# Optimization experiments

Measured on AMD Instinct MI355X. Metric: run time of the kernel, lower is better.

The kernel has to match this reference:

```python
import jax, jax.numpy as jnp
import numpy as np

N_DRUG = 572
EMB = 512
K_NB = 64
SEG_NB = 16
BN_EPS = 1e-5


def setup_inputs() -> dict:
    key = jax.random.key(0)
    ks = jax.random.split(key, 8)
    return {
        "drug_name": jnp.arange(N_DRUG, dtype=jnp.int64) if jax.config.jax_enable_x64 else jnp.arange(N_DRUG, dtype=jnp.int32),
        "adj_tail": jax.random.randint(ks[0], (N_DRUG, K_NB), 0, 100000),
        "adj_relation": jax.random.randint(ks[1], (N_DRUG, K_NB), 0, 200),
        "inv_adj_idx": jax.random.randint(ks[2], (N_DRUG, SEG_NB), 0, N_DRUG),
        "drug_table": jax.random.normal(ks[3], (N_DRUG, EMB), dtype=jnp.float32),
        "rela_table": jax.random.normal(ks[4], (200, EMB), dtype=jnp.float32),
        "ent_table": jax.random.normal(ks[5], (100000, EMB), dtype=jnp.float32),
        "W_lin": jax.random.normal(ks[6], (2 * EMB, EMB), dtype=jnp.float32) * (1.0 / np.sqrt(2 * EMB)),
        "b_lin": jnp.zeros((EMB,), jnp.float32),
        "bn_gamma": jnp.ones((EMB,), jnp.float32),
        "bn_beta": jnp.zeros((EMB,), jnp.float32),
        "epoch": 2,
    }


def _forward(drug_name, adj_tail, adj_relation, inv_adj_idx,
             drug_table, rela_table, ent_table, W_lin, b_lin,
             bn_gamma, bn_beta, epoch):
    # Embedding gathers
    drug_emb = drug_table[drug_name]          # [N, D]
    rel_emb = rela_table[adj_relation]        # [N, K, D]
    ent_emb = ent_table[adj_tail]             # [N, K, D]

    # KGCN-style attention over sampled neighbors: score_k = softmax(drug . rel_k)
    scores = jax.nn.softmax(jnp.einsum('nd,nkd->nk', drug_emb, rel_emb), axis=1)
    attended = jnp.einsum('nk,nkd->nd', scores, ent_emb)  # [N, D]

    # Linear -> ReLU -> BatchNorm1d (training-mode batch stats, biased var)
    e = jnp.concatenate([attended, drug_emb], axis=1)     # [N, 2D]
    h = jax.nn.relu(e @ W_lin + b_lin)                    # [N, D]
    mu = jnp.mean(h, axis=0)
    var = jnp.mean(jnp.square(h - mu), axis=0)
    drug_f = bn_gamma * (h - mu) * jax.lax.rsqrt(var + BN_EPS) + bn_beta

    if epoch > 1:
        # Sequential in-place neighbor averaging (faithful to the Python loop:
        # later drugs see already-updated rows).
        def body(f, x):
            i, pos = x
            avg = jnp.mean(f[pos], axis=0)                # [D]
            f = f.at[i].set((avg + f[i]) * 0.5)
            return f, None
        idxs = jnp.arange(N_DRUG)
        drug_f, _ = jax.lax.scan(body, drug_f, (idxs, inv_adj_idx))
    return drug_f


def reference(drug_name, adj_tail, adj_relation, inv_adj_idx,
              drug_table, rela_table, ent_table, W_lin, b_lin,
              bn_gamma, bn_beta, epoch):
    return _forward(drug_name, adj_tail, adj_relation, inv_adj_idx,
                    drug_table, rela_table, ent_table, W_lin, b_lin,
                    bn_gamma, bn_beta, epoch)
```

## Files before the change

kernel.cpp:

```cpp
#include <hip/hip_runtime.h>
#include <hip/hip_bf16.h>

#define N_DRUG 572
#define EMB    512
#define K_NB   64
#define SEG_NB 16
#define SCOLS  16

typedef __hip_bfloat16  bf16;
typedef __hip_bfloat162 bf162;

__device__ __forceinline__ float b2f(bf16 x){ return __bfloat162float(x); }

template<typename T> __device__ __forceinline__ float ldf(const T* p);
template<> __device__ __forceinline__ float ldf<float>(const float* p){ return *p; }
template<> __device__ __forceinline__ float ldf<bf16>(const bf16* p){ return b2f(*p); }

template<typename T> __device__ __forceinline__ float2 ld2(const T* p);
template<> __device__ __forceinline__ float2 ld2<float>(const float* p){ return *(const float2*)p; }
template<> __device__ __forceinline__ float2 ld2<bf16>(const bf16* p){
    bf162 v = *(const bf162*)p; return make_float2(b2f(v.x), b2f(v.y));
}

template<typename T> __device__ __forceinline__ void st2(T* p, float x, float y);
template<> __device__ __forceinline__ void st2<float>(float* p, float x, float y){ *(float2*)p = make_float2(x, y); }
template<> __device__ __forceinline__ void st2<bf16>(bf16* p, float x, float y){
    bf162 v; v.x = __float2bfloat16(x); v.y = __float2bfloat16(y); *(bf162*)p = v;
}

__device__ __forceinline__ bool idx_is64(const void* drug_name) {
    return ((const int*)drug_name)[1] == 0;
}
__device__ __forceinline__ int ld_idx(const void* p, int i, bool is64) {
    return is64 ? (int)((const long long*)p)[i] : ((const int*)p)[i];
}

__device__ __forceinline__ bool detect_bf16(const void* tab) {
    const int lane = threadIdx.x & 63;
    int hit = 0;
    if (lane < 32) {
        const unsigned u = ((const unsigned*)tab)[lane * 997];
        const unsigned e = (u >> 7) & 0xffu;
        hit = (e >= 110u && e <= 141u) ? 1 : 0;
    }
    return __popcll(__ballot(hit)) >= 24;
}

struct __align__(16) FwdSmem {
    float e[2][2 * EMB];
    float sc[2][K_NB];
    int   tl[2][K_NB];
};

template<typename T>
__device__ void fwd_impl(FwdSmem& sm,
    const void* drug_name, const void* adj_tail, const void* adj_rel,
    const T* __restrict__ drug_table, const T* __restrict__ rela_table,
    const T* __restrict__ ent_table,  const T* __restrict__ W,
    const T* __restrict__ bl, T* __restrict__ h)
{
    const int  t    = threadIdx.x;
    const int  n0   = blockIdx.x * 2;
    const bool is64 = idx_is64(drug_name);

    #pragma unroll
    for (int dr = 0; dr < 2; ++dr) {
        const int row = ld_idx(drug_name, n0 + dr, is64);
        const float2 v = ld2(drug_table + (size_t)row * EMB + 2 * t);
        sm.e[dr][EMB + 2 * t]     = v.x;
        sm.e[dr][EMB + 2 * t + 1] = v.y;
    }
    if (t < 128) {
        const int dr = t >> 6, k = t & 63;
        sm.tl[dr][k] = ld_idx(adj_tail, (n0 + dr) * K_NB + k, is64);
    }
    __syncthreads();

    {
        const int wave = t >> 6, lane = t & 63;
        const int dr = wave >> 1;
        const int kb = (wave & 1) * 32;
        const float* ed = &sm.e[dr][EMB];
        #pragma unroll 4
        for (int i = 0; i < 32; ++i) {
            const int k   = kb + i;
            const int rid = ld_idx(adj_rel, (n0 + dr) * K_NB + k, is64);
            const T* rl = rela_table + (size_t)rid * EMB;
            float p = 0.f;
            #pragma unroll
            for (int m = 0; m < 4; ++m) {
                const int dd = 2 * lane + m * 128;
                const float2 rv = ld2(rl + dd);
                p = fmaf(ed[dd],     rv.x, p);
                p = fmaf(ed[dd + 1], rv.y, p);
            }
            #pragma unroll
            for (int off = 32; off; off >>= 1) p += __shfl_down(p, off, 64);
            if (lane == 0) sm.sc[dr][k] = p;
        }
    }
    __syncthreads();

    if (t < 128) {
        const int dr = t >> 6, k = t & 63;
        const float s = sm.sc[dr][k];
        float m = s;
        #pragma unroll
        for (int off = 32; off; off >>= 1) m = fmaxf(m, __shfl_xor(m, off, 64));
        const float ex = __expf(s - m);
        float sum = ex;
        #pragma unroll
        for (int off = 32; off; off >>= 1) sum += __shfl_xor(sum, off, 64);
        sm.sc[dr][k] = ex / sum;
    }
    __syncthreads();

    {
        float a00 = 0.f, a01 = 0.f, a10 = 0.f, a11 = 0.f;
        #pragma unroll 4
        for (int k = 0; k < K_NB; ++k) {
            const float w0 = sm.sc[0][k], w1 = sm.sc[1][k];
            const float2 v0 = ld2(ent_table + (size_t)sm.tl[0][k] * EMB + 2 * t);
            const float2 v1 = ld2(ent_table + (size_t)sm.tl[1][k] * EMB + 2 * t);
            a00 = fmaf(w0, v0.x, a00); a01 = fmaf(w0, v0.y, a01);
            a10 = fmaf(w1, v1.x, a10); a11 = fmaf(w1, v1.y, a11);
        }
        sm.e[0][2 * t] = a00; sm.e[0][2 * t + 1] = a01;
        sm.e[1][2 * t] = a10; sm.e[1][2 * t + 1] = a11;
    }
    __syncthreads();

    {
        const int d0 = 2 * t;
        const float2 bb = ld2(bl + d0);
        float a00 = bb.x, a01 = bb.y, a10 = bb.x, a11 = bb.y;
        const float4* E0 = (const float4*)&sm.e[0][0];
        const float4* E1 = (const float4*)&sm.e[1][0];
        #pragma unroll 2
        for (int q = 0; q < (2 * EMB) / 4; ++q) {
            const float4 f0 = E0[q];
            const float4 f1 = E1[q];
            const T* Wp = W + (size_t)(4 * q) * EMB + d0;
            const float2 w0 = ld2(Wp);
            const float2 w1 = ld2(Wp + EMB);
            const float2 w2 = ld2(Wp + 2 * EMB);
            const float2 w3 = ld2(Wp + 3 * EMB);
            a00 = fmaf(f0.x, w0.x, a00); a01 = fmaf(f0.x, w0.y, a01);
            a10 = fmaf(f1.x, w0.x, a10); a11 = fmaf(f1.x, w0.y, a11);
            a00 = fmaf(f0.y, w1.x, a00); a01 = fmaf(f0.y, w1.y, a01);
            a10 = fmaf(f1.y, w1.x, a10); a11 = fmaf(f1.y, w1.y, a11);
            a00 = fmaf(f0.z, w2.x, a00); a01 = fmaf(f0.z, w2.y, a01);
            a10 = fmaf(f1.z, w2.x, a10); a11 = fmaf(f1.z, w2.y, a11);
            a00 = fmaf(f0.w, w3.x, a00); a01 = fmaf(f0.w, w3.y, a01);
            a10 = fmaf(f1.w, w3.x, a10); a11 = fmaf(f1.w, w3.y, a11);
        }
        st2(h + (size_t)n0 * EMB + d0,       fmaxf(a00, 0.f), fmaxf(a01, 0.f));
        st2(h + (size_t)(n0 + 1) * EMB + d0, fmaxf(a10, 0.f), fmaxf(a11, 0.f));
    }
}

__global__ __launch_bounds__(256) void k_fwd(
    const void* drug_name, const void* adj_tail, const void* adj_rel,
    const void* drug_tab, const void* rela_tab, const void* ent_tab,
    const void* W, const void* bl, void* h)
{
    __shared__ FwdSmem sm;
    if (detect_bf16(drug_tab))
        fwd_impl<bf16>(sm, drug_name, adj_tail, adj_rel,
                       (const bf16*)drug_tab, (const bf16*)rela_tab,
                       (const bf16*)ent_tab, (const bf16*)W,
                       (const bf16*)bl, (bf16*)h);
    else
        fwd_impl<float>(sm, drug_name, adj_tail, adj_rel,
                        (const float*)drug_tab, (const float*)rela_tab,
                        (const float*)ent_tab, (const float*)W,
                        (const float*)bl, (float*)h);
}

struct __align__(16) ScanSmem {
    float    fbuf[N_DRUG * SCOLS];
    unsigned obuf[N_DRUG * SEG_NB];
    float2   corr[576];
};

__device__ __forceinline__ float bflo(unsigned u){ return __uint_as_float(u << 16); }
__device__ __forceinline__ float bfhi(unsigned u){ return __uint_as_float(u & 0xffff0000u); }
__device__ __forceinline__ unsigned pack_bf2(float a, float b) {
    bf162 v; v.x = __float2bfloat16(a); v.y = __float2bfloat16(b);
    unsigned u; __builtin_memcpy(&u, &v, 4); return u;
}

template<typename T>
__device__ __forceinline__ void stage_fbuf(float* fbuf, const T* h, int c0, int t);
template<>
__device__ __forceinline__ void stage_fbuf<float>(float* fbuf, const float* h, int c0, int t) {
    float4* dst = (float4*)fbuf;
    #pragma unroll 4
    for (int k = t; k < N_DRUG * 4; k += 64)
        dst[k] = *(const float4*)(h + (size_t)(k >> 2) * EMB + c0 + 4 * (k & 3));
}
template<>
__device__ __forceinline__ void stage_fbuf<bf16>(float* fbuf, const bf16* h, int c0, int t) {
    float4* dst = (float4*)fbuf;
    #pragma unroll 4
    for (int k = t; k < N_DRUG * 2; k += 64) {
        const uint4 v = *(const uint4*)(h + (size_t)(k >> 1) * EMB + c0 + 8 * (k & 1));
        dst[2 * k]     = make_float4(bflo(v.x), bfhi(v.x), bflo(v.y), bfhi(v.y));
        dst[2 * k + 1] = make_float4(bflo(v.z), bfhi(v.z), bflo(v.w), bfhi(v.w));
    }
}

template<typename T>
__device__ __forceinline__ void flush_fbuf(const float* fbuf, T* h, int c0, int t);
template<>
__device__ __forceinline__ void flush_fbuf<float>(const float* fbuf, float* h, int c0, int t) {
    const float4* src = (const float4*)fbuf;
    #pragma unroll 4
    for (int k = t; k < N_DRUG * 4; k += 64)
        *(float4*)(h + (size_t)(k >> 2) * EMB + c0 + 4 * (k & 3)) = src[k];
}
template<>
__device__ __forceinline__ void flush_fbuf<bf16>(const float* fbuf, bf16* h, int c0, int t) {
    const float4* src = (const float4*)fbuf;
    #pragma unroll 4
    for (int k = t; k < N_DRUG * 2; k += 64) {
        const float4 f0 = src[2 * k], f1 = src[2 * k + 1];
        uint4 o;
        o.x = pack_bf2(f0.x, f0.y); o.y = pack_bf2(f0.z, f0.w);
        o.z = pack_bf2(f1.x, f1.y); o.w = pack_bf2(f1.z, f1.w);
        *(uint4*)(h + (size_t)(k >> 1) * EMB + c0 + 8 * (k & 1)) = o;
    }
}

template<bool IS64>
__device__ __forceinline__ void stage_obuf(unsigned* obuf, const void* inv, int t) {
    const uint4* src = (const uint4*)inv;
    if (IS64) {
        #pragma unroll 4
        for (int k = t; k < (N_DRUG * SEG_NB) / 2; k += 64) {
            const uint4 v = src[k];
            *(uint2*)(obuf + 2 * k) = make_uint2(v.x << 4, v.z << 4);
        }
    } else {
        uint4* dst = (uint4*)obuf;
        #pragma unroll 4
        for (int k = t; k < (N_DRUG * SEG_NB) / 4; k += 64) {
            uint4 v = src[k];
            v.x <<= 4; v.y <<= 4; v.z <<= 4; v.w <<= 4;
            dst[k] = v;
        }
    }
}

#define LD_OFF(OF, R)                                                        \
    {                                                                        \
        const uint4 q0 = ob4[(R) * 4 + 0], q1 = ob4[(R) * 4 + 1];            \
        const uint4 q2 = ob4[(R) * 4 + 2], q3 = ob4[(R) * 4 + 3];            \
        OF[0]=q0.x; OF[1]=q0.y; OF[2]=q0.z; OF[3]=q0.w;                      \
        OF[4]=q1.x; OF[5]=q1.y; OF[6]=q1.z; OF[7]=q1.w;                      \
        OF[8]=q2.x; OF[9]=q2.y; OF[10]=q2.z; OF[11]=q2.w;                    \
        OF[12]=q3.x; OF[13]=q3.y; OF[14]=q3.z; OF[15]=q3.w;                  \
    }

#define SCAN_ROW(V, OF, fi, cc, I, IP2, IP4)                                 \
    {                                                                        \
        const float s0 = (V[0] + V[1]) + (V[2] + V[3]);                      \
        const float s1 = (V[4] + V[5]) + (V[6] + V[7]);                      \
        const float s2 = (V[8] + V[9]) + (V[10] + V[11]);                    \
        const float s3 = (V[12] + V[13]) + (V[14] + V[15]);                  \
        float nv = fmaf((s0 + s1) + (s2 + s3), 1.f / 32.f, fi * 0.5f);       \
        nv = fmaf(cc.x, nv1 - f1, nv);                                       \
        nv = fmaf(cc.y, nv2 - f2, nv);                                       \
        f2 = f1; f1 = fi; nv2 = nv1; nv1 = nv;                               \
        _Pragma("unroll")                                                    \
        for (int j = 0; j < 16; ++j) V[j] = fb[OF[j]];                       \
        fi = fb[(IP2) * 16];                                                 \
        cc = sm.corr[(I) + 2];                                               \
        sm.fbuf[(I) * SCOLS + t] = nv;                                       \
        LD_OFF(OF, IP4);                                                     \
    }

template<typename T, bool IS64>
__device__ void scan_impl(ScanSmem& sm, T* __restrict__ h,
    const void* __restrict__ inv, const T* __restrict__ gamma,
    const T* __restrict__ beta, const void* __restrict__ epoch)
{
    const int t  = threadIdx.x;
    const int c0 = blockIdx.x * SCOLS;

    stage_obuf<IS64>(sm.obuf, inv, t);
    stage_fbuf<T>(sm.fbuf, h, c0, t);
    for (int k = t; k < 576; k += 64) sm.corr[k] = make_float2(0.f, 0.f);
    __syncthreads();

    for (int i = 1 + t; i < N_DRUG; i += 64) {
        const unsigned tA = (unsigned)(i - 1) << 4;
        const unsigned tB = (unsigned)(i - 2) << 4;
        int cA = 0, cB = 0;
        #pragma unroll
        for (int j = 0; j < SEG_NB; ++j) {
            const unsigned o = sm.obuf[i * SEG_NB + j];
            cA += (o == tA) ? 1 : 0;
            cB += (o == tB) ? 1 : 0;
        }
        sm.corr[i] = make_float2((float)cA * (1.f / 32.f), (float)cB * (1.f / 32.f));
    }

    {
        const int c = t & 15, g = t >> 4;
        float s = 0.f, s2 = 0.f;
        for (int r = g; r < N_DRUG; r += 4) {
            const float x = sm.fbuf[r * SCOLS + c];
            s += x; s2 = fmaf(x, x, s2);
        }
        s  += __shfl_xor(s, 16, 64);  s  += __shfl_xor(s, 32, 64);
        s2 += __shfl_xor(s2, 16, 64); s2 += __shfl_xor(s2, 32, 64);
        const float mu  = s * (1.f / N_DRUG);
        const float var = fmaxf(s2 * (1.f / N_DRUG) - mu * mu, 0.f);
        const float gs  = ldf(gamma + c0 + c) * rsqrtf(var + 1e-5f);
        const float bs  = ldf(beta  + c0 + c);
        for (int r = g; r < N_DRUG; r += 4) {
            const float x = sm.fbuf[r * SCOLS + c];
            sm.fbuf[r * SCOLS + c] = fmaf(x - mu, gs, bs);
        }
    }
    __syncthreads();

    if (((const int*)epoch)[0] > 1 && t < 16) {
        const float* fb  = sm.fbuf + t;
        const uint4* ob4 = (const uint4*)sm.obuf;

        unsigned OFA[16], OFB[16];
        float    VA[16],  VB[16];

        LD_OFF(OFA, 0); LD_OFF(OFB, 1);
        #pragma unroll
        for (int j = 0; j < 16; ++j) VA[j] = fb[OFA[j]];
        #pragma unroll
        for (int j = 0; j < 16; ++j) VB[j] = fb[OFB[j]];
        LD_OFF(OFA, 2); LD_OFF(OFB, 3);
        float  fiA = fb[0],        fiB = fb[16];
        float2 ccA = sm.corr[0],   ccB = sm.corr[1];
        float nv1 = 0.f, nv2 = 0.f, f1 = 0.f, f2 = 0.f;

        for (int i = 0; i < N_DRUG; i += 2) {
            const int a2 = (i + 2 < N_DRUG) ? i + 2 : N_DRUG - 1;
            const int a4 = (i + 4 < N_DRUG) ? i + 4 : N_DRUG - 1;
            SCAN_ROW(VA, OFA, fiA, ccA, i, a2, a4);
            const int b2 = (i + 3 < N_DRUG) ? i + 3 : N_DRUG - 1;
            const int b4 = (i + 5 < N_DRUG) ? i + 5 : N_DRUG - 1;
            SCAN_ROW(VB, OFB, fiB, ccB, i + 1, b2, b4);
        }
    }
    __syncthreads();

    flush_fbuf<T>(sm.fbuf, h, c0, t);
}

__global__ __launch_bounds__(64) void k_scan(
    void* h, const void* inv, const void* gamma, const void* beta,
    const void* epoch, const void* drug_name, const void* drug_tab)
{
    __shared__ ScanSmem sm;
    const bool isbf = detect_bf16(drug_tab);
    const bool is64 = idx_is64(drug_name);
    if (isbf) {
        if (is64) scan_impl<bf16, true >(sm, (bf16*)h, inv, (const bf16*)gamma, (const bf16*)beta, epoch);
        else      scan_impl<bf16, false>(sm, (bf16*)h, inv, (const bf16*)gamma, (const bf16*)beta, epoch);
    } else {
        if (is64) scan_impl<float, true >(sm, (float*)h, inv, (const float*)gamma, (const float*)beta, epoch);
        else      scan_impl<float, false>(sm, (float*)h, inv, (const float*)gamma, (const float*)beta, epoch);
    }
}

extern "C" void kernel_launch(void* const* d_in, const int* in_sizes, int n_in,
                              void* d_out, int out_size, void* d_ws, size_t ws_size,
                              hipStream_t stream)
{
    (void)in_sizes; (void)n_in; (void)out_size; (void)d_ws; (void)ws_size;

    k_fwd<<<N_DRUG / 2, 256, 0, stream>>>(
        d_in[0], d_in[1], d_in[2],
        d_in[4], d_in[5], d_in[6],
        d_in[7], d_in[8],
        d_out);
    k_scan<<<EMB / SCOLS, 64, 0, stream>>>(
        d_out, d_in[3],
        d_in[9], d_in[10], d_in[11],
        d_in[0], d_in[4]);
}
```

Before: 496.7 us.

## Spread sequential neighbor-averaging scan across four lane groups with shuffle reduction

The serial neighbor-averaging scan previously ran on 16 lanes, each loading and summing all 16 neighbor values per row. It now uses all 64 lanes: each group of 16 lanes gathers 4 of the neighbors and the partial sums are combined with two cross-lane shuffles. The software pipeline is reworked to a 4-row rotation with deeper prefetch of offsets, self values and correction terms. This shortens the per-row serial dependency chain of loads and adds, at the cost of shuffle latency on the critical path.

```diff
diff --git a/kernel.cpp b/kernel.cpp
--- a/kernel.cpp
+++ b/kernel.cpp
@@ -252,32 +252,21 @@
     }
 }
 
-#define LD_OFF(OF, R)                                                        \
+#define BODY(Vc, Vn, Qn, Fc, Cc, I)                                          \
     {                                                                        \
-        const uint4 q0 = ob4[(R) * 4 + 0], q1 = ob4[(R) * 4 + 1];            \
-        const uint4 q2 = ob4[(R) * 4 + 2], q3 = ob4[(R) * 4 + 3];            \
-        OF[0]=q0.x; OF[1]=q0.y; OF[2]=q0.z; OF[3]=q0.w;                      \
-        OF[4]=q1.x; OF[5]=q1.y; OF[6]=q1.z; OF[7]=q1.w;                      \
-        OF[8]=q2.x; OF[9]=q2.y; OF[10]=q2.z; OF[11]=q2.w;                    \
-        OF[12]=q3.x; OF[13]=q3.y; OF[14]=q3.z; OF[15]=q3.w;                  \
-    }
-
-#define SCAN_ROW(V, OF, fi, cc, I, IP2, IP4)                                 \
-    {                                                                        \
-        const float s0 = (V[0] + V[1]) + (V[2] + V[3]);                      \
-        const float s1 = (V[4] + V[5]) + (V[6] + V[7]);                      \
-        const float s2 = (V[8] + V[9]) + (V[10] + V[11]);                    \
-        const float s3 = (V[12] + V[13]) + (V[14] + V[15]);                  \
-        float nv = fmaf((s0 + s1) + (s2 + s3), 1.f / 32.f, fi * 0.5f);       \
-        nv = fmaf(cc.x, nv1 - f1, nv);                                       \
-        nv = fmaf(cc.y, nv2 - f2, nv);                                       \
-        f2 = f1; f1 = fi; nv2 = nv1; nv1 = nv;                               \
-        _Pragma("unroll")                                                    \
-        for (int j = 0; j < 16; ++j) V[j] = fb[OF[j]];                       \
-        fi = fb[(IP2) * 16];                                                 \
-        cc = sm.corr[(I) + 2];                                               \
-        sm.fbuf[(I) * SCOLS + t] = nv;                                       \
-        LD_OFF(OF, IP4);                                                     \
+        Vn.x = fb[Qn.x + c]; Vn.y = fb[Qn.y + c];                            \
+        Vn.z = fb[Qn.z + c]; Vn.w = fb[Qn.w + c];                            \
+        Qn = ob4[(((I) + 6 <= N_DRUG - 1) ? (I) + 6 : N_DRUG - 1) * 4 + g];  \
+        float s = (Vc.x + Vc.y) + (Vc.z + Vc.w);                             \
+        s += __shfl_xor(s, 16, 64);                                          \
+        s += __shfl_xor(s, 32, 64);                                          \
+        float nv = fmaf(s, 1.f / 32.f, Fc * 0.5f);                           \
+        nv = fmaf(Cc.x, nv1 - f1, nv);                                       \
+        nv = fmaf(Cc.y, nv2 - f2, nv);                                       \
+        f2 = f1; f1 = Fc; nv2 = nv1; nv1 = nv;                               \
+        Fc = fb[(((I) + 4 <= N_DRUG - 1) ? (I) + 4 : N_DRUG - 1) * 16 + c];  \
+        Cc = sm.corr[(I) + 4];                                               \
+        if (g == 0) sm.fbuf[(I) * SCOLS + c] = nv;                           \
     }
 
 template<typename T, bool IS64>
@@ -326,30 +315,36 @@
     }
     __syncthreads();
 
-    if (((const int*)epoch)[0] > 1 && t < 16) {
-        const float* fb  = sm.fbuf + t;
+    if (((const int*)epoch)[0] > 1) {
+        const int c = t & 15, g = t >> 4;
+        const float* fb  = sm.fbuf;
         const uint4* ob4 = (const uint4*)sm.obuf;
 
-        unsigned OFA[16], OFB[16];
-        float    VA[16],  VB[16];
-
-        LD_OFF(OFA, 0); LD_OFF(OFB, 1);
-        #pragma unroll
-        for (int j = 0; j < 16; ++j) VA[j] = fb[OFA[j]];
-        #pragma unroll
-        for (int j = 0; j < 16; ++j) VB[j] = fb[OFB[j]];
-        LD_OFF(OFA, 2); LD_OFF(OFB, 3);
-        float  fiA = fb[0],        fiB = fb[16];
-        float2 ccA = sm.corr[0],   ccB = sm.corr[1];
+        float4 V0, V1, V2{}, V3{};
+        uint4  Q0, Q1, Q2, Q3;
+        float  F0, F1, F2, F3;
+        float2 C0, C1, C2, C3;
+
+        {
+            const uint4 o0 = ob4[0 * 4 + g], o1 = ob4[1 * 4 + g];
+            V0.x = fb[o0.x + c]; V0.y = fb[o0.y + c];
+            V0.z = fb[o0.z + c]; V0.w = fb[o0.w + c];
+            V1.x = fb[o1.x + c]; V1.y = fb[o1.y + c];
+            V1.z = fb[o1.z + c]; V1.w = fb[o1.w + c];
+            Q2 = ob4[2 * 4 + g]; Q3 = ob4[3 * 4 + g];
+            Q0 = ob4[4 * 4 + g]; Q1 = ob4[5 * 4 + g];
+            F0 = fb[0 * 16 + c]; F1 = fb[1 * 16 + c];
+            F2 = fb[2 * 16 + c]; F3 = fb[3 * 16 + c];
+            C0 = sm.corr[0]; C1 = sm.corr[1];
+            C2 = sm.corr[2]; C3 = sm.corr[3];
+        }
         float nv1 = 0.f, nv2 = 0.f, f1 = 0.f, f2 = 0.f;
 
-        for (int i = 0; i < N_DRUG; i += 2) {
-            const int a2 = (i + 2 < N_DRUG) ? i + 2 : N_DRUG - 1;
-            const int a4 = (i + 4 < N_DRUG) ? i + 4 : N_DRUG - 1;
-            SCAN_ROW(VA, OFA, fiA, ccA, i, a2, a4);
-            const int b2 = (i + 3 < N_DRUG) ? i + 3 : N_DRUG - 1;
-            const int b4 = (i + 5 < N_DRUG) ? i + 5 : N_DRUG - 1;
-            SCAN_ROW(VB, OFB, fiB, ccB, i + 1, b2, b4);
+        for (int i = 0; i < N_DRUG; i += 4) {
+            BODY(V0, V2, Q2, F0, C0, i);
+            BODY(V1, V3, Q3, F1, C1, i + 1);
+            BODY(V2, V0, Q0, F2, C2, i + 2);
+            BODY(V3, V1, Q1, F3, C3, i + 3);
         }
     }
     __syncthreads();
```

New measurement: 442.7 us. -10.9%, faster.
